# Performance work log

Hardware: AMD Instinct MI355X
Metric: run time of the kernel (lower is better)

The kernel has to match this reference:

```python
import jax, jax.numpy as jnp
import numpy as np

B, T, IN, H, GAT_HEADS, MHA_HEADS, C = 32, 512, 128, 256, 4, 4, 8
OUT = H // GAT_HEADS          # 64, GAT per-head out_features
HD = H // MHA_HEADS           # 64, MHA head dim
ALPHA = 0.2                   # LeakyReLU slope
EPS = 1e-5                    # LayerNorm eps


def setup_inputs() -> dict:
    key = jax.random.key(0)
    ks = iter(jax.random.split(key, 32))
    def rn(shape, scale=0.05):
        return jax.random.normal(next(ks), shape, dtype=jnp.float32) * scale
    return {
        "x": jax.random.normal(next(ks), (B, T, IN), dtype=jnp.float32),
        # GRU layer 0 / 1 (PyTorch gate order r,z,n)
        "gru_W_ih0": rn((3 * H, IN)), "gru_W_hh0": rn((3 * H, H)),
        "gru_b_ih0": rn((3 * H,)), "gru_b_hh0": rn((3 * H,)),
        "gru_W_ih1": rn((3 * H, H)), "gru_W_hh1": rn((3 * H, H)),
        "gru_b_ih1": rn((3 * H,)), "gru_b_hh1": rn((3 * H,)),
        # GAT: per-head W [H,OUT] and additive attention vector a [2*OUT]
        "gat_W": rn((GAT_HEADS, H, OUT)), "gat_a": rn((GAT_HEADS, 2 * OUT)),
        "ln_g": jnp.ones((H,), jnp.float32), "ln_b": jnp.zeros((H,), jnp.float32),
        # MHA packed in-proj (q,k,v) + out-proj
        "mha_in_w": rn((3 * H, H)), "mha_in_b": rn((3 * H,)),
        "mha_out_w": rn((H, H)), "mha_out_b": rn((H,)),
        "fc1_w": rn((H // 2, H)), "fc1_b": rn((H // 2,)),
        "fc2_w": rn((C, H // 2)), "fc2_b": rn((C,)),
    }


def _gru_layer(x, W_ih, W_hh, b_ih, b_hh):
    # x: [B,T,D] -> hidden states [B,T,H]; PyTorch GRU cell math, gates r,z,n
    xp = jnp.einsum('btd,gd->btg', x, W_ih) + b_ih  # precompute input proj [B,T,3H]
    Hh = W_hh.shape[1]
    def step(h, xp_t):
        g = h @ W_hh.T + b_hh
        xr, xz, xn = jnp.split(xp_t, 3, axis=-1)
        hr, hz, hn = jnp.split(g, 3, axis=-1)
        r = jax.nn.sigmoid(xr + hr)
        z = jax.nn.sigmoid(xz + hz)
        n = jnp.tanh(xn + r * hn)
        h_new = (1.0 - z) * n + z * h
        return h_new, h_new
    h0 = jnp.zeros((x.shape[0], Hh), x.dtype)
    _, hs = jax.lax.scan(step, h0, jnp.swapaxes(xp, 0, 1))
    return jnp.swapaxes(hs, 0, 1)


def _gat_head(h_in, W, a):
    # Additive attention decomposed: e_ij = leakyrelu(a1.h_i + a2.h_j)
    # (exactly equals matmul(cat[h_i,h_j], a) without the [B,T,T,2*OUT] tensor)
    h = h_in @ W                       # [B,T,OUT]
    f_src = h @ a[:OUT]                # [B,T]
    f_dst = h @ a[OUT:]                # [B,T]
    e = jax.nn.leaky_relu(f_src[:, :, None] + f_dst[:, None, :], ALPHA)  # [B,T,T]
    attn = jax.nn.softmax(e, axis=-1)  # dropout is identity in eval mode
    return jnp.einsum('bij,bjd->bid', attn, h)


def _layer_norm(x, g, b):
    mu = x.mean(-1, keepdims=True)
    var = jnp.mean((x - mu) ** 2, -1, keepdims=True)
    return (x - mu) * jax.lax.rsqrt(var + EPS) * g + b


def _forward(x, gru_W_ih0, gru_W_hh0, gru_b_ih0, gru_b_hh0,
             gru_W_ih1, gru_W_hh1, gru_b_ih1, gru_b_hh1,
             gat_W, gat_a, ln_g, ln_b,
             mha_in_w, mha_in_b, mha_out_w, mha_out_b,
             fc1_w, fc1_b, fc2_w, fc2_b):
    g = _gru_layer(x, gru_W_ih0, gru_W_hh0, gru_b_ih0, gru_b_hh0)
    g = _gru_layer(g, gru_W_ih1, gru_W_hh1, gru_b_ih1, gru_b_hh1)  # [B,T,H]
    gat_out = jnp.concatenate([_gat_head(g, gat_W[i], gat_a[i]) for i in range(GAT_HEADS)], axis=-1)
    y = _layer_norm(g + gat_out, ln_g, ln_b)
    # Multihead self-attention (4 heads, eval-mode dropout = identity)
    qkv = y @ mha_in_w.T + mha_in_b
    q, k, v = jnp.split(qkv, 3, axis=-1)
    def split_heads(t):
        return t.reshape(t.shape[0], t.shape[1], MHA_HEADS, HD).transpose(0, 2, 1, 3)
    q, k, v = split_heads(q), split_heads(k), split_heads(v)
    scores = jnp.einsum('bhqd,bhkd->bhqk', q, k) / jnp.sqrt(jnp.float32(HD))
    attn = jax.nn.softmax(scores, axis=-1)
    ctx = jnp.einsum('bhqk,bhkd->bhqd', attn, v)
    ctx = ctx.transpose(0, 2, 1, 3).reshape(y.shape[0], y.shape[1], H)
    attn_out = ctx @ mha_out_w.T + mha_out_b
    pooled = attn_out.mean(axis=1)                    # [B,H]
    hid = jax.nn.relu(pooled @ fc1_w.T + fc1_b)
    return hid @ fc2_w.T + fc2_b                      # [B,C]


def reference(x, gru_W_ih0, gru_W_hh0, gru_b_ih0, gru_b_hh0,
              gru_W_ih1, gru_W_hh1, gru_b_ih1, gru_b_hh1,
              gat_W, gat_a, ln_g, ln_b,
              mha_in_w, mha_in_b, mha_out_w, mha_out_b,
              fc1_w, fc1_b, fc2_w, fc2_b):
    return _forward(x, gru_W_ih0, gru_W_hh0, gru_b_ih0, gru_b_hh0,
                    gru_W_ih1, gru_W_hh1, gru_b_ih1, gru_b_hh1,
                    gat_W, gat_a, ln_g, ln_b,
                    mha_in_w, mha_in_b, mha_out_w, mha_out_b,
                    fc1_w, fc1_b, fc2_w, fc2_b)
```

## Files before the change

kernel.cpp:

```cpp
#include <hip/hip_runtime.h>
#include <math.h>

#define BB 32
#define TT 512
#define INF_ 128
#define HH 256
#define H3 768
#define NHEADS 4
#define HDIM 64

typedef _Float16 half_t;
typedef half_t half2_t __attribute__((ext_vector_type(2)));
typedef half_t half4_t __attribute__((ext_vector_type(4)));
typedef half_t f16x8 __attribute__((ext_vector_type(8)));
typedef float f32x4 __attribute__((ext_vector_type(4)));

#if defined(__has_builtin)
#if __has_builtin(__builtin_amdgcn_fdot2)
#define FDOT2(a, b, c) __builtin_amdgcn_fdot2((a), (b), (c), false)
#endif
#endif
#ifndef FDOT2
#define FDOT2(a, b, c) fmaf((float)(a).x, (float)(b).x, fmaf((float)(a).y, (float)(b).y, (c)))
#endif

#define BCH(x) __builtin_bit_cast(half2_t, x)
#define PKH(a, b) __builtin_bit_cast(unsigned, half2_t{(half_t)(a), (half_t)(b)})

__device__ __forceinline__ float wsum(float v) {
#pragma unroll
  for (int o = 32; o > 0; o >>= 1) v += __shfl_xor(v, o, 64);
  return v;
}
__device__ __forceinline__ float wmax(float v) {
#pragma unroll
  for (int o = 32; o > 0; o >>= 1) v = fmaxf(v, __shfl_xor(v, o, 64));
  return v;
}

__global__ void castk(const float* __restrict__ s, half_t* __restrict__ d, int n) {
  int i = (blockIdx.x * 256 + threadIdx.x) * 4;
  if (i < n) {
    float4 v = *(const float4*)(s + i);
    half4_t o = {(half_t)v.x, (half_t)v.y, (half_t)v.z, (half_t)v.w};
    *(half4_t*)(d + i) = o;
  }
}

__global__ __launch_bounds__(256) void gemm_f16(
    const half_t* __restrict__ A, const half_t* __restrict__ B,
    const float* __restrict__ bias, float* __restrict__ C,
    int M, int N, int K) {
  __shared__ __align__(16) half_t As[128][40];
  __shared__ __align__(16) half_t Bs[64][40];
  const int tid = threadIdx.x;
  const int wave = tid >> 6, lane = tid & 63;
  const int m0 = blockIdx.y * 128, n0 = blockIdx.x * 64;
  const int mrow = lane & 15, quad = lane >> 4;
  f32x4 acc00 = {0.f, 0.f, 0.f, 0.f}, acc01 = acc00, acc02 = acc00, acc03 = acc00;
  f32x4 acc10 = acc00, acc11 = acc00, acc12 = acc00, acc13 = acc00;
  for (int k0 = 0; k0 < K; k0 += 32) {
    __syncthreads();
#pragma unroll
    for (int u = 0; u < 2; ++u) {
      int idx = tid + u * 256;
      int row = idx >> 2, seg = idx & 3;
      *(f16x8*)&As[row][seg * 8] =
          *(const f16x8*)&A[(size_t)(m0 + row) * K + k0 + seg * 8];
    }
    {
      int row = tid >> 2, seg = tid & 3;
      *(f16x8*)&Bs[row][seg * 8] =
          *(const f16x8*)&B[(size_t)(n0 + row) * K + k0 + seg * 8];
    }
    __syncthreads();
    f16x8 af0 = *(const f16x8*)&As[wave * 32 + mrow][quad * 8];
    f16x8 af1 = *(const f16x8*)&As[wave * 32 + 16 + mrow][quad * 8];
    f16x8 bf0 = *(const f16x8*)&Bs[mrow][quad * 8];
    f16x8 bf1 = *(const f16x8*)&Bs[16 + mrow][quad * 8];
    f16x8 bf2 = *(const f16x8*)&Bs[32 + mrow][quad * 8];
    f16x8 bf3 = *(const f16x8*)&Bs[48 + mrow][quad * 8];
    acc00 = __builtin_amdgcn_mfma_f32_16x16x32_f16(af0, bf0, acc00, 0, 0, 0);
    acc01 = __builtin_amdgcn_mfma_f32_16x16x32_f16(af0, bf1, acc01, 0, 0, 0);
    acc02 = __builtin_amdgcn_mfma_f32_16x16x32_f16(af0, bf2, acc02, 0, 0, 0);
    acc03 = __builtin_amdgcn_mfma_f32_16x16x32_f16(af0, bf3, acc03, 0, 0, 0);
    acc10 = __builtin_amdgcn_mfma_f32_16x16x32_f16(af1, bf0, acc10, 0, 0, 0);
    acc11 = __builtin_amdgcn_mfma_f32_16x16x32_f16(af1, bf1, acc11, 0, 0, 0);
    acc12 = __builtin_amdgcn_mfma_f32_16x16x32_f16(af1, bf2, acc12, 0, 0, 0);
    acc13 = __builtin_amdgcn_mfma_f32_16x16x32_f16(af1, bf3, acc13, 0, 0, 0);
  }
  float bv0 = bias ? bias[n0 + mrow] : 0.f;
  float bv1 = bias ? bias[n0 + 16 + mrow] : 0.f;
  float bv2 = bias ? bias[n0 + 32 + mrow] : 0.f;
  float bv3 = bias ? bias[n0 + 48 + mrow] : 0.f;
  const int rb = m0 + wave * 32 + quad * 4;
#pragma unroll
  for (int r = 0; r < 4; ++r) {
    float* c0 = C + (size_t)(rb + r) * N + n0;
    c0[mrow] = acc00[r] + bv0;
    c0[16 + mrow] = acc01[r] + bv1;
    c0[32 + mrow] = acc02[r] + bv2;
    c0[48 + mrow] = acc03[r] + bv3;
    float* c1 = C + (size_t)(rb + 16 + r) * N + n0;
    c1[mrow] = acc10[r] + bv0;
    c1[16 + mrow] = acc11[r] + bv1;
    c1[32 + mrow] = acc12[r] + bv2;
    c1[48 + mrow] = acc13[r] + bv3;
  }
}

#define LDW(g, p, a, b, i)                             \
  {                                                    \
    float4 v = (p)[i];                                 \
    g##a = half2_t{(half_t)v.x, (half_t)v.y};          \
    g##b = half2_t{(half_t)v.z, (half_t)v.w};          \
  }
#define LDW28(g, p)                                                        \
  LDW(g, p, 0, 1, 0) LDW(g, p, 2, 3, 1) LDW(g, p, 4, 5, 2)                 \
  LDW(g, p, 6, 7, 3) LDW(g, p, 8, 9, 4) LDW(g, p, 10, 11, 5)               \
  LDW(g, p, 12, 13, 6) LDW(g, p, 14, 15, 7) LDW(g, p, 16, 17, 8)           \
  LDW(g, p, 18, 19, 9) LDW(g, p, 20, 21, 10) LDW(g, p, 22, 23, 11)         \
  LDW(g, p, 24, 25, 12) LDW(g, p, 26, 27, 13) LDW(g, p, 28, 29, 14)        \
  LDW(g, p, 30, 31, 15) LDW(g, p, 32, 33, 16) LDW(g, p, 34, 35, 17)        \
  LDW(g, p, 36, 37, 18) LDW(g, p, 38, 39, 19) LDW(g, p, 40, 41, 20)        \
  LDW(g, p, 42, 43, 21) LDW(g, p, 44, 45, 22) LDW(g, p, 46, 47, 23)        \
  LDW(g, p, 48, 49, 24) LDW(g, p, 50, 51, 25) LDW(g, p, 52, 53, 26)        \
  LDW(g, p, 54, 55, 27)

#define DECL56(g)                                                          \
  half2_t g##0, g##1, g##2, g##3, g##4, g##5, g##6, g##7, g##8, g##9,      \
      g##10, g##11, g##12, g##13, g##14, g##15, g##16, g##17, g##18,       \
      g##19, g##20, g##21, g##22, g##23, g##24, g##25, g##26, g##27,       \
      g##28, g##29, g##30, g##31, g##32, g##33, g##34, g##35, g##36,       \
      g##37, g##38, g##39, g##40, g##41, g##42, g##43, g##44, g##45,       \
      g##46, g##47, g##48, g##49, g##50, g##51, g##52, g##53, g##54, g##55;

#define CHA(c8, a0, a1, a2, a3)                                            \
  {                                                                        \
    float4 v = hp4[c8];                                                    \
    uint4 nv = WSq[((c8)-1) * 512 + tid];                                  \
    half2_t t0 = __builtin_bit_cast(half2_t, v.x);                         \
    half2_t t1 = __builtin_bit_cast(half2_t, v.y);                         \
    half2_t t2 = __builtin_bit_cast(half2_t, v.z);                         \
    half2_t t3 = __builtin_bit_cast(half2_t, v.w);                         \
    ar = FDOT2(wr##a0, t0, ar); az = FDOT2(wz##a0, t0, az); an = FDOT2(BCH(nv.x), t0, an); \
    ar = FDOT2(wr##a1, t1, ar); az = FDOT2(wz##a1, t1, az); an = FDOT2(BCH(nv.y), t1, an); \
    ar = FDOT2(wr##a2, t2, ar); az = FDOT2(wz##a2, t2, az); an = FDOT2(BCH(nv.z), t2, an); \
    ar = FDOT2(wr##a3, t3, ar); az = FDOT2(wz##a3, t3, az); an = FDOT2(BCH(nv.w), t3, an); \
  }

#define CHB(c8)                                                            \
  {                                                                        \
    float4 v = hp4[c8];                                                    \
    uint4 nv = WSq[((c8)-1) * 512 + tid];                                  \
    uint4 rv = WSq[(15 + ((c8)-14)) * 512 + tid];                          \
    uint4 zv = WSq[(17 + ((c8)-14)) * 512 + tid];                          \
    half2_t t0 = __builtin_bit_cast(half2_t, v.x);                         \
    half2_t t1 = __builtin_bit_cast(half2_t, v.y);                         \
    half2_t t2 = __builtin_bit_cast(half2_t, v.z);                         \
    half2_t t3 = __builtin_bit_cast(half2_t, v.w);                         \
    ar = FDOT2(BCH(rv.x), t0, ar); az = FDOT2(BCH(zv.x), t0, az); an = FDOT2(BCH(nv.x), t0, an); \
    ar = FDOT2(BCH(rv.y), t1, ar); az = FDOT2(BCH(zv.y), t1, az); an = FDOT2(BCH(nv.y), t1, an); \
    ar = FDOT2(BCH(rv.z), t2, ar); az = FDOT2(BCH(zv.z), t2, az); an = FDOT2(BCH(nv.z), t2, an); \
    ar = FDOT2(BCH(rv.w), t3, ar); az = FDOT2(BCH(zv.w), t3, az); an = FDOT2(BCH(nv.w), t3, an); \
  }

__device__ __forceinline__ uint4 pk8(const float* p) {
  float4 a = *(const float4*)p;
  float4 b = *(const float4*)(p + 4);
  return uint4{PKH(a.x, a.y), PKH(a.z, a.w), PKH(b.x, b.y), PKH(b.z, b.w)};
}

__global__ __launch_bounds__(512) void gru_layer(
    const float* __restrict__ xp, const float* __restrict__ Whh,
    const float* __restrict__ bhh, float* __restrict__ out,
    half_t* __restrict__ out16) {
  __shared__ __align__(16) uint4 WSq[19 * 512];
  __shared__ __align__(16) half_t hs[2][2][144];
  const int tid = threadIdx.x;
  const int kh = tid & 1, j = tid >> 1;
  const int b = blockIdx.x;
  const bool wf32 = (out != nullptr);
  DECL56(wr)
  DECL56(wz)
  half2_t wn0, wn1, wn2, wn3;
  {
    const float4* pr = (const float4*)(Whh + (size_t)j * HH + kh * 128);
    const float4* pz = (const float4*)(Whh + (size_t)(HH + j) * HH + kh * 128);
    const float4* pn = (const float4*)(Whh + (size_t)(2 * HH + j) * HH + kh * 128);
    LDW28(wr, pr)
    LDW28(wz, pz)
    LDW(wn, pn, 0, 1, 0)
    LDW(wn, pn, 2, 3, 1)
  }
  {
    const float* rowN = Whh + (size_t)(2 * HH + j) * HH + kh * 128;
    const float* rowR = Whh + (size_t)j * HH + kh * 128;
    const float* rowZ = Whh + (size_t)(HH + j) * HH + kh * 128;
#pragma unroll
    for (int sg = 0; sg < 15; ++sg) WSq[sg * 512 + tid] = pk8(rowN + 8 + 8 * sg);
#pragma unroll
    for (int sg = 0; sg < 2; ++sg) WSq[(15 + sg) * 512 + tid] = pk8(rowR + 112 + 8 * sg);
#pragma unroll
    for (int sg = 0; sg < 2; ++sg) WSq[(17 + sg) * 512 + tid] = pk8(rowZ + 112 + 8 * sg);
  }
  const float br = bhh[j], bz = bhh[HH + j], bn = bhh[2 * HH + j];
  for (int i = tid; i < 288; i += 512) ((unsigned*)hs)[i] = 0u;
  __syncthreads();
  float hprev = 0.f;
  const float* xrow = xp + (size_t)b * TT * H3;
  float* orow = out + (size_t)b * TT * HH;
  half_t* orow16 = out16 + (size_t)b * TT * HH;
  for (int t = 0; t < TT; ++t) {
    float xr = xrow[j], xz = xrow[HH + j], xn = xrow[2 * HH + j];
    const float4* hp4 = (const float4*)&hs[t & 1][kh][0];
    float ar = 0.f, az = 0.f, an = 0.f;
    {
      float4 v = hp4[0];
      half2_t t0 = __builtin_bit_cast(half2_t, v.x);
      half2_t t1 = __builtin_bit_cast(half2_t, v.y);
      half2_t t2 = __builtin_bit_cast(half2_t, v.z);
      half2_t t3 = __builtin_bit_cast(half2_t, v.w);
      ar = FDOT2(wr0, t0, ar); az = FDOT2(wz0, t0, az); an = FDOT2(wn0, t0, an);
      ar = FDOT2(wr1, t1, ar); az = FDOT2(wz1, t1, az); an = FDOT2(wn1, t1, an);
      ar = FDOT2(wr2, t2, ar); az = FDOT2(wz2, t2, az); an = FDOT2(wn2, t2, an);
      ar = FDOT2(wr3, t3, ar); az = FDOT2(wz3, t3, az); an = FDOT2(wn3, t3, an);
    }
    CHA(1, 4, 5, 6, 7)
    CHA(2, 8, 9, 10, 11)
    CHA(3, 12, 13, 14, 15)
    CHA(4, 16, 17, 18, 19)
    CHA(5, 20, 21, 22, 23)
    CHA(6, 24, 25, 26, 27)
    CHA(7, 28, 29, 30, 31)
    CHA(8, 32, 33, 34, 35)
    CHA(9, 36, 37, 38, 39)
    CHA(10, 40, 41, 42, 43)
    CHA(11, 44, 45, 46, 47)
    CHA(12, 48, 49, 50, 51)
    CHA(13, 52, 53, 54, 55)
    CHB(14)
    CHB(15)
    ar += __shfl_xor(ar, 1);
    az += __shfl_xor(az, 1);
    an += __shfl_xor(an, 1);
    float rg = 1.f / (1.f + __expf(-(xr + ar + br)));
    float zg = 1.f / (1.f + __expf(-(xz + az + bz)));
    float ng = 2.f / (1.f + __expf(-2.f * (xn + rg * (an + bn)))) - 1.f;
    float hnew = (1.f - zg) * ng + zg * hprev;
    hprev = hnew;
    float hpart = __shfl_xor(hnew, 2);
    if ((tid & 3) == 0) {
      half2_t pk;
      pk.x = (half_t)hnew;
      pk.y = (half_t)hpart;
      *(half2_t*)&hs[(t + 1) & 1][j >> 7][j & 127] = pk;
    }
    if (kh == 0) {
      orow16[j] = (half_t)hnew;
      if (wf32) orow[j] = hnew;
    }
    __syncthreads();
    xrow += H3;
    orow += HH;
    orow16 += HH;
  }
}

__global__ void gat_wt(const float* __restrict__ W, half_t* __restrict__ Wt) {
  int idx = blockIdx.x * 256 + threadIdx.x;
  int col = idx >> 8, k = idx & 255;
  Wt[idx] = (half_t)W[((size_t)((col >> 6) * HH + k)) * HDIM + (col & 63)];
}

__global__ void gat_fsd(const float* __restrict__ hgat, const float* __restrict__ a,
                        float* __restrict__ fsrc, float* __restrict__ fdst) {
  int b = blockIdx.x, hd = blockIdx.y, t = threadIdx.x;
  const float* hp = hgat + ((size_t)(b * TT + t)) * HH + hd * HDIM;
  const float* ap = a + hd * 2 * HDIM;
  float fs = 0.f, fd = 0.f;
#pragma unroll 4
  for (int d = 0; d < HDIM; ++d) {
    float hv = hp[d];
    fs += hv * ap[d];
    fd += hv * ap[HDIM + d];
  }
  fsrc[(b * NHEADS + hd) * TT + t] = fs;
  fdst[(b * NHEADS + hd) * TT + t] = fd;
}

__global__ __launch_bounds__(256) void gat_attn(
    const float* __restrict__ hgat, const float* __restrict__ fsrc,
    const float* __restrict__ fdst, float* __restrict__ out) {
  __shared__ __align__(16) float Ht[128][64];
  __shared__ __align__(16) float fd[128];
  __shared__ __align__(16) float pq[4][128][8];
  const int tid = threadIdx.x, wave = tid >> 6, lane = tid & 63;
  const int hd = blockIdx.y, b = blockIdx.z;
  const int i0 = blockIdx.x * 32 + wave * 8;
  const float* fs = fsrc + (size_t)(b * NHEADS + hd) * TT;
  const float* fdp = fdst + (size_t)(b * NHEADS + hd) * TT;
  float m[8], l[8], acc[8], fi[8];
#pragma unroll
  for (int q = 0; q < 8; ++q) { m[q] = -1e30f; l[q] = 0.f; acc[q] = 0.f; fi[q] = fs[i0 + q]; }
  for (int jt = 0; jt < TT; jt += 128) {
#pragma unroll
    for (int u = 0; u < 8; ++u) {
      int idx = tid + u * 256;
      int jj = idx >> 4, dq = (idx & 15) * 4;
      *(float4*)&Ht[jj][dq] =
          *(const float4*)&hgat[((size_t)(b * TT + jt + jj)) * HH + hd * HDIM + dq];
    }
    if (tid < 128) fd[tid] = fdp[jt + tid];
    __syncthreads();
#pragma unroll
    for (int q = 0; q < 8; ++q) {
      float e0 = fi[q] + fd[lane];      e0 = (e0 > 0.f) ? e0 : 0.2f * e0;
      float e1 = fi[q] + fd[lane + 64]; e1 = (e1 > 0.f) ? e1 : 0.2f * e1;
      float mn = fmaxf(m[q], wmax(fmaxf(e0, e1)));
      float corr = __expf(m[q] - mn);
      float p0 = __expf(e0 - mn), p1 = __expf(e1 - mn);
      l[q] = l[q] * corr + wsum(p0 + p1);
      m[q] = mn;
      acc[q] *= corr;
      pq[wave][lane][q] = p0;
      pq[wave][lane + 64][q] = p1;
    }
#pragma unroll 4
    for (int jj = 0; jj < 128; ++jj) {
      float4 pa = *(const float4*)&pq[wave][jj][0];
      float4 pb = *(const float4*)&pq[wave][jj][4];
      float hv = Ht[jj][lane];
      acc[0] += pa.x * hv; acc[1] += pa.y * hv; acc[2] += pa.z * hv; acc[3] += pa.w * hv;
      acc[4] += pb.x * hv; acc[5] += pb.y * hv; acc[6] += pb.z * hv; acc[7] += pb.w * hv;
    }
    __syncthreads();
  }
#pragma unroll
  for (int q = 0; q < 8; ++q)
    out[((size_t)(b * TT + i0 + q)) * HH + hd * HDIM + lane] = acc[q] / l[q];
}

__global__ __launch_bounds__(256) void ln_res(
    const float* __restrict__ g, const float* __restrict__ gat,
    const float* __restrict__ gamma, const float* __restrict__ beta,
    half_t* __restrict__ y16) {
  int wave = threadIdx.x >> 6, lane = threadIdx.x & 63;
  size_t n = (size_t)blockIdx.x * 4 + wave;
  float4 v = ((const float4*)(g + n * HH))[lane];
  float4 w = ((const float4*)(gat + n * HH))[lane];
  v.x += w.x; v.y += w.y; v.z += w.z; v.w += w.w;
  float mu = wsum(v.x + v.y + v.z + v.w) * (1.f / 256.f);
  float dx = v.x - mu, dy = v.y - mu, dz = v.z - mu, dw = v.w - mu;
  float var = wsum(dx * dx + dy * dy + dz * dz + dw * dw) * (1.f / 256.f);
  float rstd = rsqrtf(var + 1e-5f);
  float4 gm = ((const float4*)gamma)[lane];
  float4 bt = ((const float4*)beta)[lane];
  half4_t o = {(half_t)(dx * rstd * gm.x + bt.x), (half_t)(dy * rstd * gm.y + bt.y),
               (half_t)(dz * rstd * gm.z + bt.z), (half_t)(dw * rstd * gm.w + bt.w)};
  ((half4_t*)(y16 + n * HH))[lane] = o;
}

__global__ __launch_bounds__(256) void mha_attn(const float* __restrict__ qkv,
                                                half_t* __restrict__ ctx16) {
  __shared__ __align__(16) float KV[8320];
  __shared__ __align__(16) float qq[4][64][8];
  __shared__ __align__(16) float pq[4][128][8];
  const int tid = threadIdx.x, wave = tid >> 6, lane = tid & 63;
  const int hd = blockIdx.y, b = blockIdx.z;
  const int i0 = blockIdx.x * 32 + wave * 8;
#pragma unroll
  for (int q = 0; q < 8; ++q)
    qq[wave][lane][q] = qkv[((size_t)(b * TT + i0 + q)) * H3 + hd * HDIM + lane];
  float m[8], l[8], acc[8];
#pragma unroll
  for (int q = 0; q < 8; ++q) { m[q] = -1e30f; l[q] = 0.f; acc[q] = 0.f; }
  for (int jt = 0; jt < TT; jt += 128) {
#pragma unroll
    for (int u = 0; u < 8; ++u) {
      int idx = tid + u * 256;
      int jj = idx >> 4, dq = (idx & 15) * 4;
      float4 kv = *(const float4*)&qkv[((size_t)(b * TT + jt + jj)) * H3 + HH + hd * HDIM + dq];
      KV[(dq + 0) * 130 + jj] = kv.x;
      KV[(dq + 1) * 130 + jj] = kv.y;
      KV[(dq + 2) * 130 + jj] = kv.z;
      KV[(dq + 3) * 130 + jj] = kv.w;
    }
    __syncthreads();
    float e0[8] = {}, e1[8] = {};
#pragma unroll 8
    for (int dd = 0; dd < 64; ++dd) {
      float4 qa = *(const float4*)&qq[wave][dd][0];
      float4 qb = *(const float4*)&qq[wave][dd][4];
      float k0 = KV[dd * 130 + lane], k1 = KV[dd * 130 + 64 + lane];
      e0[0] += qa.x * k0; e0[1] += qa.y * k0; e0[2] += qa.z * k0; e0[3] += qa.w * k0;
      e0[4] += qb.x * k0; e0[5] += qb.y * k0; e0[6] += qb.z * k0; e0[7] += qb.w * k0;
      e1[0] += qa.x * k1; e1[1] += qa.y * k1; e1[2] += qa.z * k1; e1[3] += qa.w * k1;
      e1[4] += qb.x * k1; e1[5] += qb.y * k1; e1[6] += qb.z * k1; e1[7] += qb.w * k1;
    }
    __syncthreads();
#pragma unroll
    for (int u = 0; u < 8; ++u) {
      int idx = tid + u * 256;
      int jj = idx >> 4, dq = (idx & 15) * 4;
      *(float4*)&KV[jj * 64 + dq] =
          *(const float4*)&qkv[((size_t)(b * TT + jt + jj)) * H3 + 2 * HH + hd * HDIM + dq];
    }
#pragma unroll
    for (int q = 0; q < 8; ++q) {
      float s0 = e0[q] * 0.125f, s1 = e1[q] * 0.125f;
      float mn = fmaxf(m[q], wmax(fmaxf(s0, s1)));
      float corr = __expf(m[q] - mn);
      float p0 = __expf(s0 - mn), p1 = __expf(s1 - mn);
      l[q] = l[q] * corr + wsum(p0 + p1);
      m[q] = mn;
      acc[q] *= corr;
      pq[wave][lane][q] = p0;
      pq[wave][lane + 64][q] = p1;
    }
    __syncthreads();
#pragma unroll 4
    for (int jj = 0; jj < 128; ++jj) {
      float4 pa = *(const float4*)&pq[wave][jj][0];
      float4 pb = *(const float4*)&pq[wave][jj][4];
      float hv = KV[jj * 64 + lane];
      acc[0] += pa.x * hv; acc[1] += pa.y * hv; acc[2] += pa.z * hv; acc[3] += pa.w * hv;
      acc[4] += pb.x * hv; acc[5] += pb.y * hv; acc[6] += pb.z * hv; acc[7] += pb.w * hv;
    }
    __syncthreads();
  }
#pragma unroll
  for (int q = 0; q < 8; ++q)
    ctx16[((size_t)(b * TT + i0 + q)) * HH + hd * HDIM + lane] = (half_t)(acc[q] / l[q]);
}

__global__ void mean_pool(const float* __restrict__ x, float* __restrict__ out) {
  int b = blockIdx.x, j = threadIdx.x;
  const float* p = x + (size_t)b * TT * HH + j;
  float s = 0.f;
  for (int t = 0; t < TT; ++t) s += p[(size_t)t * HH];
  out[b * HH + j] = s * (1.f / 512.f);
}

__global__ void fc1_k(const float* __restrict__ pooled, const float* __restrict__ w,
                      const float* __restrict__ bias, float* __restrict__ hid) {
  int b = blockIdx.x, o = threadIdx.x;
  const float* pp = pooled + b * HH;
  const float* wp = w + o * HH;
  float s = 0.f;
#pragma unroll 4
  for (int k = 0; k < HH; ++k) s += pp[k] * wp[k];
  hid[b * 128 + o] = fmaxf(s + bias[o], 0.f);
}

__global__ void fc2_k(const float* __restrict__ hid, const float* __restrict__ w,
                      const float* __restrict__ bias, float* __restrict__ out) {
  int t = threadIdx.x;
  int mm = t >> 3, c = t & 7;
  const float* hp = hid + mm * 128;
  const float* wp = w + c * 128;
  float s = 0.f;
#pragma unroll 4
  for (int k = 0; k < 128; ++k) s += hp[k] * wp[k];
  out[mm * 8 + c] = s + bias[c];
}

extern "C" void kernel_launch(void* const* d_in, const int* in_sizes, int n_in,
                              void* d_out, int out_size, void* d_ws, size_t ws_size,
                              hipStream_t stream) {
  (void)in_sizes; (void)n_in; (void)out_size; (void)ws_size;
  const float* x    = (const float*)d_in[0];
  const float* Wih0 = (const float*)d_in[1];
  const float* Whh0 = (const float*)d_in[2];
  const float* bih0 = (const float*)d_in[3];
  const float* bhh0 = (const float*)d_in[4];
  const float* Wih1 = (const float*)d_in[5];
  const float* Whh1 = (const float*)d_in[6];
  const float* bih1 = (const float*)d_in[7];
  const float* bhh1 = (const float*)d_in[8];
  const float* gatW = (const float*)d_in[9];
  const float* gatA = (const float*)d_in[10];
  const float* lng  = (const float*)d_in[11];
  const float* lnb  = (const float*)d_in[12];
  const float* inw  = (const float*)d_in[13];
  const float* inb  = (const float*)d_in[14];
  const float* outw = (const float*)d_in[15];
  const float* outb = (const float*)d_in[16];
  const float* f1w  = (const float*)d_in[17];
  const float* f1b  = (const float*)d_in[18];
  const float* f2w  = (const float*)d_in[19];
  const float* f2b  = (const float*)d_in[20];
  float* out = (float*)d_out;
  float* ws = (float*)d_ws;

  float* XPA   = ws;
  float* G0    = ws + 12582912;
  float* G1    = G0 + 4194304;
  float* Yb    = G1 + 4194304;
  float* HGAT  = Yb + 4194304;
  float* GATWTf= HGAT + 4194304;
  float* FSRC  = GATWTf + 65536;
  float* FDST  = FSRC + 65536;
  float* POOL  = FDST + 65536;
  float* HIDb  = POOL + 8192;
  float* W16b  = HIDb + 4096;

  half_t* X16     = (half_t*)G1;
  half_t* G0_16   = (half_t*)Yb;
  half_t* G1_16   = (half_t*)(Yb + 2097152);
  half_t* CTX16   = (half_t*)HGAT;
  half_t* Y16     = (half_t*)(HGAT + 2097152);
  half_t* GATWT16 = (half_t*)GATWTf;
  half_t* W16ih0  = (half_t*)W16b;
  half_t* W16ih1  = (half_t*)(W16b + 49152);
  half_t* W16in   = (half_t*)(W16b + 49152 + 98304);
  half_t* W16out  = (half_t*)(W16b + 49152 + 98304 + 98304);

  castk<<<2048, 256, 0, stream>>>(x, X16, 2097152);
  castk<<<96, 256, 0, stream>>>(Wih0, W16ih0, 98304);
  castk<<<192, 256, 0, stream>>>(Wih1, W16ih1, 196608);
  castk<<<192, 256, 0, stream>>>(inw, W16in, 196608);
  castk<<<64, 256, 0, stream>>>(outw, W16out, 65536);
  gat_wt<<<256, 256, 0, stream>>>(gatW, GATWT16);
  gemm_f16<<<dim3(12, 128), 256, 0, stream>>>(X16, W16ih0, bih0, XPA, 16384, 768, 128);
  gru_layer<<<32, 512, 0, stream>>>(XPA, Whh0, bhh0, nullptr, G0_16);
  gemm_f16<<<dim3(12, 128), 256, 0, stream>>>(G0_16, W16ih1, bih1, XPA, 16384, 768, 256);
  gru_layer<<<32, 512, 0, stream>>>(XPA, Whh1, bhh1, G1, G1_16);
  gemm_f16<<<dim3(4, 128), 256, 0, stream>>>(G1_16, GATWT16, nullptr, HGAT, 16384, 256, 256);
  gat_fsd<<<dim3(32, 4), 512, 0, stream>>>(HGAT, gatA, FSRC, FDST);
  gat_attn<<<dim3(16, 4, 32), 256, 0, stream>>>(HGAT, FSRC, FDST, G0);
  ln_res<<<4096, 256, 0, stream>>>(G1, G0, lng, lnb, Y16);
  gemm_f16<<<dim3(12, 128), 256, 0, stream>>>(Y16, W16in, inb, XPA, 16384, 768, 256);
  mha_attn<<<dim3(16, 4, 32), 256, 0, stream>>>(XPA, CTX16);
  gemm_f16<<<dim3(4, 128), 256, 0, stream>>>(CTX16, W16out, outb, Yb, 16384, 256, 256);
  mean_pool<<<32, 256, 0, stream>>>(Yb, POOL);
  fc1_k<<<32, 128, 0, stream>>>(POOL, f1w, f1b, HIDb);
  fc2_k<<<1, 256, 0, stream>>>(HIDb, f2w, f2b, out);
}
```

Baseline: 1.933 ms.

## Compute GRU recurrent matvec with MFMA and register-resident f16 weights

```diff
diff --git a/kernel.cpp b/kernel.cpp
--- a/kernel.cpp
+++ b/kernel.cpp
@@ -14,18 +14,6 @@
 typedef half_t half4_t __attribute__((ext_vector_type(4)));
 typedef half_t f16x8 __attribute__((ext_vector_type(8)));
 typedef float f32x4 __attribute__((ext_vector_type(4)));
-
-#if defined(__has_builtin)
-#if __has_builtin(__builtin_amdgcn_fdot2)
-#define FDOT2(a, b, c) __builtin_amdgcn_fdot2((a), (b), (c), false)
-#endif
-#endif
-#ifndef FDOT2
-#define FDOT2(a, b, c) fmaf((float)(a).x, (float)(b).x, fmaf((float)(a).y, (float)(b).y, (c)))
-#endif
-
-#define BCH(x) __builtin_bit_cast(half2_t, x)
-#define PKH(a, b) __builtin_bit_cast(unsigned, half2_t{(half_t)(a), (half_t)(b)})
 
 __device__ __forceinline__ float wsum(float v) {
 #pragma unroll
@@ -109,161 +97,102 @@
   }
 }
 
-#define LDW(g, p, a, b, i)                             \
-  {                                                    \
-    float4 v = (p)[i];                                 \
-    g##a = half2_t{(half_t)v.x, (half_t)v.y};          \
-    g##b = half2_t{(half_t)v.z, (half_t)v.w};          \
-  }
-#define LDW28(g, p)                                                        \
-  LDW(g, p, 0, 1, 0) LDW(g, p, 2, 3, 1) LDW(g, p, 4, 5, 2)                 \
-  LDW(g, p, 6, 7, 3) LDW(g, p, 8, 9, 4) LDW(g, p, 10, 11, 5)               \
-  LDW(g, p, 12, 13, 6) LDW(g, p, 14, 15, 7) LDW(g, p, 16, 17, 8)           \
-  LDW(g, p, 18, 19, 9) LDW(g, p, 20, 21, 10) LDW(g, p, 22, 23, 11)         \
-  LDW(g, p, 24, 25, 12) LDW(g, p, 26, 27, 13) LDW(g, p, 28, 29, 14)        \
-  LDW(g, p, 30, 31, 15) LDW(g, p, 32, 33, 16) LDW(g, p, 34, 35, 17)        \
-  LDW(g, p, 36, 37, 18) LDW(g, p, 38, 39, 19) LDW(g, p, 40, 41, 20)        \
-  LDW(g, p, 42, 43, 21) LDW(g, p, 44, 45, 22) LDW(g, p, 46, 47, 23)        \
-  LDW(g, p, 48, 49, 24) LDW(g, p, 50, 51, 25) LDW(g, p, 52, 53, 26)        \
-  LDW(g, p, 54, 55, 27)
-
-#define DECL56(g)                                                          \
-  half2_t g##0, g##1, g##2, g##3, g##4, g##5, g##6, g##7, g##8, g##9,      \
-      g##10, g##11, g##12, g##13, g##14, g##15, g##16, g##17, g##18,       \
-      g##19, g##20, g##21, g##22, g##23, g##24, g##25, g##26, g##27,       \
-      g##28, g##29, g##30, g##31, g##32, g##33, g##34, g##35, g##36,       \
-      g##37, g##38, g##39, g##40, g##41, g##42, g##43, g##44, g##45,       \
-      g##46, g##47, g##48, g##49, g##50, g##51, g##52, g##53, g##54, g##55;
-
-#define CHA(c8, a0, a1, a2, a3)                                            \
-  {                                                                        \
-    float4 v = hp4[c8];                                                    \
-    uint4 nv = WSq[((c8)-1) * 512 + tid];                                  \
-    half2_t t0 = __builtin_bit_cast(half2_t, v.x);                         \
-    half2_t t1 = __builtin_bit_cast(half2_t, v.y);                         \
-    half2_t t2 = __builtin_bit_cast(half2_t, v.z);                         \
-    half2_t t3 = __builtin_bit_cast(half2_t, v.w);                         \
-    ar = FDOT2(wr##a0, t0, ar); az = FDOT2(wz##a0, t0, az); an = FDOT2(BCH(nv.x), t0, an); \
-    ar = FDOT2(wr##a1, t1, ar); az = FDOT2(wz##a1, t1, az); an = FDOT2(BCH(nv.y), t1, an); \
-    ar = FDOT2(wr##a2, t2, ar); az = FDOT2(wz##a2, t2, az); an = FDOT2(BCH(nv.z), t2, an); \
-    ar = FDOT2(wr##a3, t3, ar); az = FDOT2(wz##a3, t3, az); an = FDOT2(BCH(nv.w), t3, an); \
-  }
-
-#define CHB(c8)                                                            \
-  {                                                                        \
-    float4 v = hp4[c8];                                                    \
-    uint4 nv = WSq[((c8)-1) * 512 + tid];                                  \
-    uint4 rv = WSq[(15 + ((c8)-14)) * 512 + tid];                          \
-    uint4 zv = WSq[(17 + ((c8)-14)) * 512 + tid];                          \
-    half2_t t0 = __builtin_bit_cast(half2_t, v.x);                         \
-    half2_t t1 = __builtin_bit_cast(half2_t, v.y);                         \
-    half2_t t2 = __builtin_bit_cast(half2_t, v.z);                         \
-    half2_t t3 = __builtin_bit_cast(half2_t, v.w);                         \
-    ar = FDOT2(BCH(rv.x), t0, ar); az = FDOT2(BCH(zv.x), t0, az); an = FDOT2(BCH(nv.x), t0, an); \
-    ar = FDOT2(BCH(rv.y), t1, ar); az = FDOT2(BCH(zv.y), t1, az); an = FDOT2(BCH(nv.y), t1, an); \
-    ar = FDOT2(BCH(rv.z), t2, ar); az = FDOT2(BCH(zv.z), t2, az); an = FDOT2(BCH(nv.z), t2, an); \
-    ar = FDOT2(BCH(rv.w), t3, ar); az = FDOT2(BCH(zv.w), t3, az); an = FDOT2(BCH(nv.w), t3, an); \
-  }
-
-__device__ __forceinline__ uint4 pk8(const float* p) {
+__device__ __forceinline__ f16x8 ldw8(const float* p) {
   float4 a = *(const float4*)p;
   float4 b = *(const float4*)(p + 4);
-  return uint4{PKH(a.x, a.y), PKH(a.z, a.w), PKH(b.x, b.y), PKH(b.z, b.w)};
-}
-
-__global__ __launch_bounds__(512) void gru_layer(
+  return f16x8{(half_t)a.x, (half_t)a.y, (half_t)a.z, (half_t)a.w,
+               (half_t)b.x, (half_t)b.y, (half_t)b.z, (half_t)b.w};
+}
+
+#define WDECL(nt) f16x8 w##nt##_0, w##nt##_1, w##nt##_2, w##nt##_3, \
+                        w##nt##_4, w##nt##_5, w##nt##_6, w##nt##_7;
+#define WLOAD(nt)                                                          \
+  {                                                                        \
+    const float* wr = Whh + (size_t)(64 * w + 16 * nt + col) * HH + quad * 8; \
+    w##nt##_0 = ldw8(wr + 0 * 32);                                         \
+    w##nt##_1 = ldw8(wr + 1 * 32);                                         \
+    w##nt##_2 = ldw8(wr + 2 * 32);                                         \
+    w##nt##_3 = ldw8(wr + 3 * 32);                                         \
+    w##nt##_4 = ldw8(wr + 4 * 32);                                         \
+    w##nt##_5 = ldw8(wr + 5 * 32);                                         \
+    w##nt##_6 = ldw8(wr + 6 * 32);                                         \
+    w##nt##_7 = ldw8(wr + 7 * 32);                                         \
+  }
+#define MSTEP(ak, kt)                                                        \
+  acc0 = __builtin_amdgcn_mfma_f32_16x16x32_f16(ak, w0_##kt, acc0, 0, 0, 0); \
+  acc1 = __builtin_amdgcn_mfma_f32_16x16x32_f16(ak, w1_##kt, acc1, 0, 0, 0); \
+  acc2 = __builtin_amdgcn_mfma_f32_16x16x32_f16(ak, w2_##kt, acc2, 0, 0, 0); \
+  acc3 = __builtin_amdgcn_mfma_f32_16x16x32_f16(ak, w3_##kt, acc3, 0, 0, 0);
+
+__global__ __launch_bounds__(768) void gru_layer(
     const float* __restrict__ xp, const float* __restrict__ Whh,
     const float* __restrict__ bhh, float* __restrict__ out,
     half_t* __restrict__ out16) {
-  __shared__ __align__(16) uint4 WSq[19 * 512];
-  __shared__ __align__(16) half_t hs[2][2][144];
+  __shared__ __align__(16) half_t hs[2][256];
+  __shared__ __align__(16) float gbuf[768];
   const int tid = threadIdx.x;
-  const int kh = tid & 1, j = tid >> 1;
+  const int w = tid >> 6, lane = tid & 63;
+  const int col = lane & 15, quad = lane >> 4;
   const int b = blockIdx.x;
   const bool wf32 = (out != nullptr);
-  DECL56(wr)
-  DECL56(wz)
-  half2_t wn0, wn1, wn2, wn3;
-  {
-    const float4* pr = (const float4*)(Whh + (size_t)j * HH + kh * 128);
-    const float4* pz = (const float4*)(Whh + (size_t)(HH + j) * HH + kh * 128);
-    const float4* pn = (const float4*)(Whh + (size_t)(2 * HH + j) * HH + kh * 128);
-    LDW28(wr, pr)
-    LDW28(wz, pz)
-    LDW(wn, pn, 0, 1, 0)
-    LDW(wn, pn, 2, 3, 1)
-  }
-  {
-    const float* rowN = Whh + (size_t)(2 * HH + j) * HH + kh * 128;
-    const float* rowR = Whh + (size_t)j * HH + kh * 128;
-    const float* rowZ = Whh + (size_t)(HH + j) * HH + kh * 128;
-#pragma unroll
-    for (int sg = 0; sg < 15; ++sg) WSq[sg * 512 + tid] = pk8(rowN + 8 + 8 * sg);
-#pragma unroll
-    for (int sg = 0; sg < 2; ++sg) WSq[(15 + sg) * 512 + tid] = pk8(rowR + 112 + 8 * sg);
-#pragma unroll
-    for (int sg = 0; sg < 2; ++sg) WSq[(17 + sg) * 512 + tid] = pk8(rowZ + 112 + 8 * sg);
-  }
-  const float br = bhh[j], bz = bhh[HH + j], bn = bhh[2 * HH + j];
-  for (int i = tid; i < 288; i += 512) ((unsigned*)hs)[i] = 0u;
+
+  WDECL(0) WDECL(1) WDECL(2) WDECL(3)
+  WLOAD(0) WLOAD(1) WLOAD(2) WLOAD(3)
+
+  float br = 0.f, bz = 0.f, bn = 0.f, hprev = 0.f;
+  if (tid < 256) {
+    br = bhh[tid];
+    bz = bhh[HH + tid];
+    bn = bhh[2 * HH + tid];
+    hs[0][tid] = (half_t)0.f;
+  }
   __syncthreads();
-  float hprev = 0.f;
+
   const float* xrow = xp + (size_t)b * TT * H3;
-  float* orow = out + (size_t)b * TT * HH;
   half_t* orow16 = out16 + (size_t)b * TT * HH;
+  float* orow = wf32 ? out + (size_t)b * TT * HH : nullptr;
+
   for (int t = 0; t < TT; ++t) {
-    float xr = xrow[j], xz = xrow[HH + j], xn = xrow[2 * HH + j];
-    const float4* hp4 = (const float4*)&hs[t & 1][kh][0];
-    float ar = 0.f, az = 0.f, an = 0.f;
-    {
-      float4 v = hp4[0];
-      half2_t t0 = __builtin_bit_cast(half2_t, v.x);
-      half2_t t1 = __builtin_bit_cast(half2_t, v.y);
-      half2_t t2 = __builtin_bit_cast(half2_t, v.z);
-      half2_t t3 = __builtin_bit_cast(half2_t, v.w);
-      ar = FDOT2(wr0, t0, ar); az = FDOT2(wz0, t0, az); an = FDOT2(wn0, t0, an);
-      ar = FDOT2(wr1, t1, ar); az = FDOT2(wz1, t1, az); an = FDOT2(wn1, t1, an);
-      ar = FDOT2(wr2, t2, ar); az = FDOT2(wz2, t2, az); an = FDOT2(wn2, t2, an);
-      ar = FDOT2(wr3, t3, ar); az = FDOT2(wz3, t3, az); an = FDOT2(wn3, t3, an);
-    }
-    CHA(1, 4, 5, 6, 7)
-    CHA(2, 8, 9, 10, 11)
-    CHA(3, 12, 13, 14, 15)
-    CHA(4, 16, 17, 18, 19)
-    CHA(5, 20, 21, 22, 23)
-    CHA(6, 24, 25, 26, 27)
-    CHA(7, 28, 29, 30, 31)
-    CHA(8, 32, 33, 34, 35)
-    CHA(9, 36, 37, 38, 39)
-    CHA(10, 40, 41, 42, 43)
-    CHA(11, 44, 45, 46, 47)
-    CHA(12, 48, 49, 50, 51)
-    CHA(13, 52, 53, 54, 55)
-    CHB(14)
-    CHB(15)
-    ar += __shfl_xor(ar, 1);
-    az += __shfl_xor(az, 1);
-    an += __shfl_xor(an, 1);
-    float rg = 1.f / (1.f + __expf(-(xr + ar + br)));
-    float zg = 1.f / (1.f + __expf(-(xz + az + bz)));
-    float ng = 2.f / (1.f + __expf(-2.f * (xn + rg * (an + bn)))) - 1.f;
-    float hnew = (1.f - zg) * ng + zg * hprev;
-    hprev = hnew;
-    float hpart = __shfl_xor(hnew, 2);
-    if ((tid & 3) == 0) {
-      half2_t pk;
-      pk.x = (half_t)hnew;
-      pk.y = (half_t)hpart;
-      *(half2_t*)&hs[(t + 1) & 1][j >> 7][j & 127] = pk;
-    }
-    if (kh == 0) {
-      orow16[j] = (half_t)hnew;
-      if (wf32) orow[j] = hnew;
+    float xr = 0.f, xz = 0.f, xn = 0.f;
+    if (tid < 256) {
+      xr = xrow[tid];
+      xz = xrow[HH + tid];
+      xn = xrow[2 * HH + tid];
+    }
+    const half_t* hb = &hs[t & 1][quad * 8];
+    f16x8 a0 = *(const f16x8*)(hb + 0 * 32);
+    f16x8 a1 = *(const f16x8*)(hb + 1 * 32);
+    f16x8 a2 = *(const f16x8*)(hb + 2 * 32);
+    f16x8 a3 = *(const f16x8*)(hb + 3 * 32);
+    f16x8 a4 = *(const f16x8*)(hb + 4 * 32);
+    f16x8 a5 = *(const f16x8*)(hb + 5 * 32);
+    f16x8 a6 = *(const f16x8*)(hb + 6 * 32);
+    f16x8 a7 = *(const f16x8*)(hb + 7 * 32);
+    f32x4 acc0 = {0.f, 0.f, 0.f, 0.f}, acc1 = acc0, acc2 = acc0, acc3 = acc0;
+    MSTEP(a0, 0) MSTEP(a1, 1) MSTEP(a2, 2) MSTEP(a3, 3)
+    MSTEP(a4, 4) MSTEP(a5, 5) MSTEP(a6, 6) MSTEP(a7, 7)
+    if (lane < 16) {
+      gbuf[64 * w + lane] = acc0[0];
+      gbuf[64 * w + 16 + lane] = acc1[0];
+      gbuf[64 * w + 32 + lane] = acc2[0];
+      gbuf[64 * w + 48 + lane] = acc3[0];
+    }
+    __syncthreads();
+    if (tid < 256) {
+      float ar = gbuf[tid], az = gbuf[HH + tid], an = gbuf[2 * HH + tid];
+      float rg = 1.f / (1.f + __expf(-(xr + ar + br)));
+      float zg = 1.f / (1.f + __expf(-(xz + az + bz)));
+      float ng = 2.f / (1.f + __expf(-2.f * (xn + rg * (an + bn)))) - 1.f;
+      float hnew = (1.f - zg) * ng + zg * hprev;
+      hprev = hnew;
+      hs[(t + 1) & 1][tid] = (half_t)hnew;
+      orow16[tid] = (half_t)hnew;
+      if (wf32) orow[tid] = hnew;
     }
     __syncthreads();
     xrow += H3;
-    orow += HH;
     orow16 += HH;
+    if (wf32) orow += HH;
   }
 }
 
@@ -523,9 +452,9 @@
   castk<<<64, 256, 0, stream>>>(outw, W16out, 65536);
   gat_wt<<<256, 256, 0, stream>>>(gatW, GATWT16);
   gemm_f16<<<dim3(12, 128), 256, 0, stream>>>(X16, W16ih0, bih0, XPA, 16384, 768, 128);
-  gru_layer<<<32, 512, 0, stream>>>(XPA, Whh0, bhh0, nullptr, G0_16);
+  gru_layer<<<32, 768, 0, stream>>>(XPA, Whh0, bhh0, nullptr, G0_16);
   gemm_f16<<<dim3(12, 128), 256, 0, stream>>>(G0_16, W16ih1, bih1, XPA, 16384, 768, 256);
-  gru_layer<<<32, 512, 0, stream>>>(XPA, Whh1, bhh1, G1, G1_16);
+  gru_layer<<<32, 768, 0, stream>>>(XPA, Whh1, bhh1, G1, G1_16);
   gemm_f16<<<dim3(4, 128), 256, 0, stream>>>(G1_16, GATWT16, nullptr, HGAT, 16384, 256, 256);
   gat_fsd<<<dim3(32, 4), 512, 0, stream>>>(HGAT, gatA, FSRC, FDST);
   gat_attn<<<dim3(16, 4, 32), 256, 0, stream>>>(HGAT, FSRC, FDST, G0);
```

After: 2.295 ms. 1.19x slower.
